# Optimization experiments

Measured on AMD Instinct MI355X. Metric: run time of the kernel, lower is better.

The kernel has to match this reference:

```python
import jax, jax.numpy as jnp
import numpy as np

N = 100000   # nodes
E = 800000   # undirected (unique) edges; directed count = 2*E
DV = 128; DE = 16; DH = 128; DO = 128
G = 64       # graphs in batch


def setup_inputs() -> dict:
    key = jax.random.key(0)
    ks = jax.random.split(key, 8)
    x = jax.random.normal(ks[0], (N, DV), jnp.float32)
    edge_index = jax.random.randint(ks[1], (2, 2 * E), 0, N, dtype=jnp.int32)
    edge_attr = jax.random.normal(ks[2], (E, DE), jnp.float32)
    batch = jnp.sort(jax.random.randint(ks[3], (N,), 0, G, dtype=jnp.int32))
    s = lambda k, shp, fan: jax.random.normal(k, shp, jnp.float32) / np.sqrt(fan)
    W_gcn = s(ks[4], (DV, DH), DV); b_gcn = jnp.zeros((DH,), jnp.float32)
    W_le = s(ks[5], (DE, DH), DE); b_le = jnp.zeros((DH,), jnp.float32)
    W_lin = s(ks[6], (2 * DH, DH), 2 * DH); b_lin = jnp.zeros((DH,), jnp.float32)
    W_out = s(ks[7], (DH, DO), DH); b_out = jnp.zeros((DO,), jnp.float32)
    return dict(x=x, edge_index=edge_index, edge_attr=edge_attr, batch=batch,
                W_gcn=W_gcn, b_gcn=b_gcn, W_le=W_le, b_le=b_le,
                W_lin=W_lin, b_lin=b_lin, W_out=W_out, b_out=b_out)


def reference(x, edge_index, edge_attr, batch,
              W_gcn, b_gcn, W_le, b_le, W_lin, b_lin, W_out, b_out):
    n = x.shape[0]
    loop = jnp.arange(n, dtype=edge_index.dtype)
    src = jnp.concatenate([edge_index[0], loop])  # [2E+N] with self loops
    dst = jnp.concatenate([edge_index[1], loop])

    # ---- GCNConv: symmetric norm, self-loops, lin then aggregate, + bias ----
    xw = x @ W_gcn                                      # [N, DH]
    ones_e = jnp.ones(src.shape[0], jnp.float32)
    deg = jax.ops.segment_sum(ones_e, dst, num_segments=n)  # >=1 via self loops
    dinv = jax.lax.rsqrt(deg)
    norm = dinv[src] * dinv[dst]                        # [2E+N]
    h = jax.ops.segment_sum(norm[:, None] * xw[src], dst, num_segments=n) + b_gcn
    h = jax.nn.relu(h)

    # ---- EdgeGCN: duplicate edge_attr per direction, self-loop attr = ones ----
    ea2 = jnp.repeat(edge_attr, 2, axis=0)              # [2E, DE] interleaved
    ea_full = jnp.concatenate([ea2, jnp.ones((n, edge_attr.shape[1]), jnp.float32)])
    edge_feat = ea_full @ W_le + b_le                   # [2E+N, DH]
    x_j = h[src]                                        # gather source node feats
    msg = jnp.concatenate([x_j, edge_feat], axis=-1) @ W_lin + b_lin
    h2 = jax.ops.segment_sum(msg, dst, num_segments=n)  # aggr='add'
    h2 = jax.nn.relu(h2)

    # ---- global mean pool + final linear ----
    cnt = jax.ops.segment_sum(jnp.ones(n, jnp.float32), batch, num_segments=G)
    pooled = jax.ops.segment_sum(h2, batch, num_segments=G) / jnp.maximum(cnt, 1.0)[:, None]
    return pooled @ W_out + b_out                       # [G, DO]
```

## Files before the change

kernel.cpp:

```cpp
#include <hip/hip_runtime.h>
#include <hip/hip_bf16.h>
#include <cstddef>

typedef unsigned int  u32;
typedef unsigned short u16;
typedef __attribute__((ext_vector_type(8))) short short8;
typedef __attribute__((ext_vector_type(4))) float f32x4;
typedef __attribute__((ext_vector_type(2))) float f32x2;

#define DV 128
#define DH 128
#define DE 16
#define DO 128
#define PSUB 32

__device__ inline float bf_lo(u32 u){ return __uint_as_float(u << 16); }
__device__ inline float bf_hi(u32 u){ return __uint_as_float(u & 0xFFFF0000u); }
__device__ inline u32 fpack2(float a, float b){
  u32 ua = __float_as_uint(a), ub = __float_as_uint(b);
  ua += 0x7FFFu + ((ua >> 16) & 1u);
  ub += 0x7FFFu + ((ub >> 16) & 1u);
  return (ua >> 16) | (ub & 0xFFFF0000u);
}
__device__ inline u16 f2bf(float a){
  u32 ua = __float_as_uint(a); ua += 0x7FFFu + ((ua >> 16) & 1u); return (u16)(ua >> 16);
}

__device__ inline void acc_fp8(u32 s, float& a0, float& a1, float& a2, float& a3){
  f32x2 lo = __builtin_amdgcn_cvt_pk_f32_fp8((int)s, false);
  f32x2 hi = __builtin_amdgcn_cvt_pk_f32_fp8((int)s, true);
  a0 += lo.x; a1 += lo.y; a2 += hi.x; a3 += hi.y;
}
__device__ inline u32 pack_fp8(float a0, float a1, float a2, float a3){
  int o = __builtin_amdgcn_cvt_pk_fp8_f32(a0, a1, 0, false);
  o = __builtin_amdgcn_cvt_pk_fp8_f32(a2, a3, o, true);
  return (u32)o;
}

__global__ void k_init(int* cnt, int n){
  int v = blockIdx.x * blockDim.x + threadIdx.x;
  if (v < n) cnt[v] = 0;
}
__global__ void k_count(const int* dst, int* cnt, int* rank, int e2){
  int j = blockIdx.x * blockDim.x + threadIdx.x;
  if (j < e2) rank[j] = atomicAdd(&cnt[dst[j]], 1);
}
__global__ __launch_bounds__(256) void k_scan1(const int* cnt, int* partial, int* bsums, int n){
  __shared__ int lds[256];
  int t = threadIdx.x;
  int base = blockIdx.x * 1024 + t * 4;
  int v0=0,v1=0,v2=0,v3=0;
  if (base + 3 < n){ int4 q = *(const int4*)(cnt + base); v0=q.x; v1=q.y; v2=q.z; v3=q.w; }
  else {
    if (base + 0 < n) v0 = cnt[base];
    if (base + 1 < n) v1 = cnt[base+1];
    if (base + 2 < n) v2 = cnt[base+2];
  }
  v0 = (v0 + 7) & ~7; v1 = (v1 + 7) & ~7; v2 = (v2 + 7) & ~7; v3 = (v3 + 7) & ~7;
  v1 += v0; v2 += v1; v3 += v2;
  lds[t] = v3; __syncthreads();
  for (int off = 1; off < 256; off <<= 1){
    int x = (t >= off) ? lds[t - off] : 0;
    __syncthreads();
    lds[t] += x;
    __syncthreads();
  }
  int add = (t > 0) ? lds[t - 1] : 0;
  if (base + 3 < n){
    int4 q; q.x = v0+add; q.y = v1+add; q.z = v2+add; q.w = v3+add;
    *(int4*)(partial + base) = q;
  } else {
    if (base + 0 < n) partial[base]   = v0 + add;
    if (base + 1 < n) partial[base+1] = v1 + add;
    if (base + 2 < n) partial[base+2] = v2 + add;
  }
  if (t == 255) bsums[blockIdx.x] = lds[255];
}
__global__ void k_scan2(const int* bsums, int* bexc, int nb){
  __shared__ int lds[128];
  int t = threadIdx.x;
  lds[t] = (t < nb) ? bsums[t] : 0;
  __syncthreads();
  for (int off = 1; off < 128; off <<= 1){
    int x = (t >= off) ? lds[t - off] : 0;
    __syncthreads();
    lds[t] += x;
    __syncthreads();
  }
  if (t < nb) bexc[t] = (t > 0) ? lds[t - 1] : 0;
}
__global__ void k_scan3(const int* partial, const int* bexc, int* row_ptr, int n){
  int i = blockIdx.x * blockDim.x + threadIdx.x;
  if (i < n) row_ptr[i + 1] = partial[i] + bexc[i >> 10];
  if (i == 0) row_ptr[0] = 0;
}
__global__ void k_prep(const int* cnt, float* dinv, float* degf, int n){
  int v = blockIdx.x * blockDim.x + threadIdx.x;
  if (v < n){
    float c = (float)(cnt[v] + 1);
    dinv[v] = rsqrtf(c);
    degf[v] = c;
  }
}
__global__ void k_scatter(const int* src, const int* dst, const int* rank,
                          const int* row_ptr, int2* ce, int e2){
  int j = blockIdx.x * blockDim.x + threadIdx.x;
  if (j < e2){
    int d = dst[j];
    int pos = row_ptr[d] + rank[j];
    ce[pos] = make_int2(src[j], j);
  }
}
__global__ void k_pad(const int* row_ptr, const int* cnt, int2* ce,
                      u32* xws_zrow, u32* h_zrow, int n){
  int v = blockIdx.x * blockDim.x + threadIdx.x;
  if (v < n){
    int s = row_ptr[v] + cnt[v], e = row_ptr[v + 1];
    for (int i = s; i < e; ++i) ce[i] = make_int2(n, 0);
  }
  if (blockIdx.x == 0 && threadIdx.x < 32){
    xws_zrow[threadIdx.x] = 0u;
    h_zrow[threadIdx.x] = 0u;
  }
}

__global__ __launch_bounds__(128) void k_wcombo(const float* W_lin, const float* b_lin,
                                                const float* W_le, const float* b_le, float* Wfull){
  int r = blockIdx.x, c = threadIdx.x;
  if (r < DH){
    Wfull[r * DH + c] = W_lin[r * DH + c];
  } else if (r < DH + DE){
    int i = r - DH;
    float acc = 0.f;
    #pragma unroll 8
    for (int k = 0; k < DH; k += 4){
      float4 wl = *(const float4*)(W_le + i * DH + k);
      acc += wl.x * W_lin[(size_t)(DH + k    ) * DH + c];
      acc += wl.y * W_lin[(size_t)(DH + k + 1) * DH + c];
      acc += wl.z * W_lin[(size_t)(DH + k + 2) * DH + c];
      acc += wl.w * W_lin[(size_t)(DH + k + 3) * DH + c];
    }
    Wfull[r * DH + c] = acc;
  } else if (r == 144){
    float acc = b_lin[c];
    #pragma unroll 8
    for (int k = 0; k < DH; k += 4){
      float4 bl = *(const float4*)(b_le + k);
      acc += bl.x * W_lin[(size_t)(DH + k    ) * DH + c];
      acc += bl.y * W_lin[(size_t)(DH + k + 1) * DH + c];
      acc += bl.z * W_lin[(size_t)(DH + k + 2) * DH + c];
      acc += bl.w * W_lin[(size_t)(DH + k + 3) * DH + c];
    }
    Wfull[r * DH + c] = acc;
  } else {
    Wfull[r * DH + c] = 0.f;
  }
}

template<int K, bool RELU, bool ABF16, bool SCALE, bool OFP8>
__global__ __launch_bounds__(256) void k_gemm_mfma(const void* Ap, const float* W, u32* outb,
                                                   const float* scale, int M){
  constexpr int SA = K + 8;
  constexpr int CS = 136;
  __shared__ u16 Wt[128 * SA];
  __shared__ u16 At[64 * SA];
  int tid = threadIdx.x;
  int row0 = blockIdx.x * 64;

  {
    int c = tid & 127, half = tid >> 7;
    for (int g = half; g < K / 8; g += 2){
      int k0 = g * 8;
      float w0 = W[(size_t)(k0+0)*128 + c], w1 = W[(size_t)(k0+1)*128 + c];
      float w2 = W[(size_t)(k0+2)*128 + c], w3 = W[(size_t)(k0+3)*128 + c];
      float w4 = W[(size_t)(k0+4)*128 + c], w5 = W[(size_t)(k0+5)*128 + c];
      float w6 = W[(size_t)(k0+6)*128 + c], w7 = W[(size_t)(k0+7)*128 + c];
      uint4 pk;
      pk.x = fpack2(w0, w1); pk.y = fpack2(w2, w3);
      pk.z = fpack2(w4, w5); pk.w = fpack2(w6, w7);
      *(uint4*)&Wt[c * SA + k0] = pk;
    }
  }
  constexpr int CH = K / 8;
  for (int idx = tid; idx < 64 * CH; idx += 256){
    int r = idx / CH, ch = idx - r * CH;
    int gr = row0 + r; if (gr > M - 1) gr = M - 1;
    uint4 pk;
    if (ABF16){
      pk = *(const uint4*)((const u16*)Ap + (size_t)gr * K + ch * 8);
    } else {
      const float* A = (const float*)Ap + (size_t)gr * K + ch * 8;
      float4 q0 = *(const float4*)A;
      float4 q1 = *(const float4*)(A + 4);
      pk.x = fpack2(q0.x, q0.y); pk.y = fpack2(q0.z, q0.w);
      pk.z = fpack2(q1.x, q1.y); pk.w = fpack2(q1.z, q1.w);
    }
    *(uint4*)&At[r * SA + ch * 8] = pk;
  }
  __syncthreads();

  int l = tid & 63, w = tid >> 6;
  int m = l & 15, quad = l >> 4;
  f32x4 acc[8];
  #pragma unroll
  for (int ct = 0; ct < 8; ++ct) acc[ct] = (f32x4){0.f, 0.f, 0.f, 0.f};
  #pragma unroll
  for (int ks = 0; ks < K; ks += 32){
    short8 av = *(const short8*)&At[(w * 16 + m) * SA + ks + quad * 8];
    #pragma unroll
    for (int ct = 0; ct < 8; ++ct){
      short8 bv = *(const short8*)&Wt[(ct * 16 + m) * SA + ks + quad * 8];
      acc[ct] = __builtin_amdgcn_mfma_f32_16x16x32_bf16(av, bv, acc[ct], 0, 0, 0);
    }
  }
  __syncthreads();

  u16* Ct = At;
  float sc[4];
  if (SCALE){
    #pragma unroll
    for (int r = 0; r < 4; ++r){
      int gr = row0 + w * 16 + quad * 4 + r;
      sc[r] = scale[gr < M ? gr : (M - 1)];
    }
  }
  #pragma unroll
  for (int ct = 0; ct < 8; ++ct){
    #pragma unroll
    for (int r = 0; r < 4; ++r){
      float vv = acc[ct][r];
      if (SCALE) vv *= sc[r];
      if (RELU)  vv = fmaxf(vv, 0.f);
      Ct[(w * 16 + quad * 4 + r) * CS + ct * 16 + m] = f2bf(vv);
    }
  }
  __syncthreads();
  if (OFP8){
    for (int idx = tid; idx < 64 * 16; idx += 256){
      int r = idx >> 4, c8 = idx & 15;
      int gr = row0 + r;
      if (gr < M){
        uint4 qv = *(const uint4*)&Ct[r * CS + c8 * 8];
        uint2 ov;
        ov.x = (u32)__builtin_amdgcn_cvt_pk_fp8_f32(bf_lo(qv.y), bf_hi(qv.y),
               __builtin_amdgcn_cvt_pk_fp8_f32(bf_lo(qv.x), bf_hi(qv.x), 0, false), true);
        ov.y = (u32)__builtin_amdgcn_cvt_pk_fp8_f32(bf_lo(qv.w), bf_hi(qv.w),
               __builtin_amdgcn_cvt_pk_fp8_f32(bf_lo(qv.z), bf_hi(qv.z), 0, false), true);
        *(uint2*)(outb + (size_t)gr * 32 + c8 * 2) = ov;
      }
    }
  } else {
    for (int idx = tid; idx < 64 * 16; idx += 256){
      int r = idx >> 4, ch = idx & 15;
      int gr = row0 + r;
      if (gr < M){
        uint4 q = *(const uint4*)&Ct[r * CS + ch * 8];
        *(uint4*)(outb + (size_t)gr * 64 + ch * 4) = q;
      }
    }
  }
}

__global__ __launch_bounds__(256) void k_phase1(const u32* xws8, const int* row_ptr, const int2* ce,
                                                const float* dinv, const float* b_gcn, u32* h8, int n){
  int lane = threadIdx.x & 63;
  int ln = lane & 31;
  int v = blockIdx.x * 8 + ((threadIdx.x >> 6) << 1) + (lane >> 5);
  if (v >= n) return;
  u32 sp = xws8[(size_t)v * 32 + ln];
  float a0 = 0.f, a1 = 0.f, a2 = 0.f, a3 = 0.f;
  acc_fp8(sp, a0, a1, a2, a3);
  int e0 = row_ptr[v], e1 = row_ptr[v + 1];
  int i = e0;
  u32 q0=0,q1=0,q2=0,q3=0,q4=0,q5=0,q6=0,q7=0;
  if (i < e1){
    const int4* cp = (const int4*)(ce + i);
    int4 A = cp[0], B = cp[1], C = cp[2], D = cp[3];
    q0 = xws8[(size_t)A.x * 32 + ln]; q1 = xws8[(size_t)A.z * 32 + ln];
    q2 = xws8[(size_t)B.x * 32 + ln]; q3 = xws8[(size_t)B.z * 32 + ln];
    q4 = xws8[(size_t)C.x * 32 + ln]; q5 = xws8[(size_t)C.z * 32 + ln];
    q6 = xws8[(size_t)D.x * 32 + ln]; q7 = xws8[(size_t)D.z * 32 + ln];
  }
  for (; i + 8 < e1; i += 8){
    const int4* cp2 = (const int4*)(ce + i + 8);
    int4 A = cp2[0], B = cp2[1], C = cp2[2], D = cp2[3];
    u32 p0 = xws8[(size_t)A.x * 32 + ln], p1 = xws8[(size_t)A.z * 32 + ln];
    u32 p2 = xws8[(size_t)B.x * 32 + ln], p3 = xws8[(size_t)B.z * 32 + ln];
    u32 p4 = xws8[(size_t)C.x * 32 + ln], p5 = xws8[(size_t)C.z * 32 + ln];
    u32 p6 = xws8[(size_t)D.x * 32 + ln], p7 = xws8[(size_t)D.z * 32 + ln];
    acc_fp8(q0, a0, a1, a2, a3); acc_fp8(q1, a0, a1, a2, a3);
    acc_fp8(q2, a0, a1, a2, a3); acc_fp8(q3, a0, a1, a2, a3);
    acc_fp8(q4, a0, a1, a2, a3); acc_fp8(q5, a0, a1, a2, a3);
    acc_fp8(q6, a0, a1, a2, a3); acc_fp8(q7, a0, a1, a2, a3);
    q0=p0; q1=p1; q2=p2; q3=p3; q4=p4; q5=p5; q6=p6; q7=p7;
  }
  if (i < e1){
    acc_fp8(q0, a0, a1, a2, a3); acc_fp8(q1, a0, a1, a2, a3);
    acc_fp8(q2, a0, a1, a2, a3); acc_fp8(q3, a0, a1, a2, a3);
    acc_fp8(q4, a0, a1, a2, a3); acc_fp8(q5, a0, a1, a2, a3);
    acc_fp8(q6, a0, a1, a2, a3); acc_fp8(q7, a0, a1, a2, a3);
  }
  float dv = dinv[v];
  float4 bg = *(const float4*)(b_gcn + ln * 4);
  a0 = fmaxf(fmaf(dv, a0, bg.x), 0.f);
  a1 = fmaxf(fmaf(dv, a1, bg.y), 0.f);
  a2 = fmaxf(fmaf(dv, a2, bg.z), 0.f);
  a3 = fmaxf(fmaf(dv, a3, bg.w), 0.f);
  h8[(size_t)v * 32 + ln] = pack_fp8(a0, a1, a2, a3);
}

__global__ __launch_bounds__(256) void k_phase2(const u32* h8, const int* row_ptr, const int2* ce,
                                                const float* edge_attr, const float* degf,
                                                u16* A2b, int n){
  int lane = threadIdx.x & 63;
  int ln = lane & 31;
  int half = lane >> 5;
  int v = blockIdx.x * 8 + ((threadIdx.x >> 6) << 1) + half;
  if (v >= n) return;
  u32 sp = h8[(size_t)v * 32 + ln];
  float a0 = 0.f, a1 = 0.f, a2 = 0.f, a3 = 0.f;
  acc_fp8(sp, a0, a1, a2, a3);
  float es = 0.f;
  int ch = ln & 15, grp = ln >> 4;
  int e0 = row_ptr[v], e1 = row_ptr[v + 1];
  int i = e0;
  u32 q0=0,q1=0,q2=0,q3=0,q4=0,q5=0,q6=0,q7=0;
  int4 A = {0,0,0,0}, B = {0,0,0,0}, C = {0,0,0,0}, D = {0,0,0,0};
  if (i < e1){
    const int4* cp = (const int4*)(ce + i);
    A = cp[0]; B = cp[1]; C = cp[2]; D = cp[3];
    q0 = h8[(size_t)A.x * 32 + ln]; q1 = h8[(size_t)A.z * 32 + ln];
    q2 = h8[(size_t)B.x * 32 + ln]; q3 = h8[(size_t)B.z * 32 + ln];
    q4 = h8[(size_t)C.x * 32 + ln]; q5 = h8[(size_t)C.z * 32 + ln];
    q6 = h8[(size_t)D.x * 32 + ln]; q7 = h8[(size_t)D.z * 32 + ln];
  }
  for (; i + 8 < e1; i += 8){
    const int4* cp2 = (const int4*)(ce + i + 8);
    int4 A2 = cp2[0], B2 = cp2[1], C2 = cp2[2], D2 = cp2[3];
    int s0x = grp ? C.x : A.x, s0y = grp ? C.y : A.y;
    int s1x = grp ? C.z : A.z, s1y = grp ? C.w : A.w;
    int s2x = grp ? D.x : B.x, s2y = grp ? D.y : B.y;
    int s3x = grp ? D.z : B.z, s3y = grp ? D.w : B.w;
    float v0 = edge_attr[(size_t)(s0y >> 1) * DE + ch];
    float v1 = edge_attr[(size_t)(s1y >> 1) * DE + ch];
    float v2 = edge_attr[(size_t)(s2y >> 1) * DE + ch];
    float v3 = edge_attr[(size_t)(s3y >> 1) * DE + ch];
    u32 p0 = h8[(size_t)A2.x * 32 + ln], p1 = h8[(size_t)A2.z * 32 + ln];
    u32 p2 = h8[(size_t)B2.x * 32 + ln], p3 = h8[(size_t)B2.z * 32 + ln];
    u32 p4 = h8[(size_t)C2.x * 32 + ln], p5 = h8[(size_t)C2.z * 32 + ln];
    u32 p6 = h8[(size_t)D2.x * 32 + ln], p7 = h8[(size_t)D2.z * 32 + ln];
    acc_fp8(q0, a0, a1, a2, a3); acc_fp8(q1, a0, a1, a2, a3);
    acc_fp8(q2, a0, a1, a2, a3); acc_fp8(q3, a0, a1, a2, a3);
    acc_fp8(q4, a0, a1, a2, a3); acc_fp8(q5, a0, a1, a2, a3);
    acc_fp8(q6, a0, a1, a2, a3); acc_fp8(q7, a0, a1, a2, a3);
    es = fmaf((s0x != n) ? 1.f : 0.f, v0, es);
    es = fmaf((s1x != n) ? 1.f : 0.f, v1, es);
    es = fmaf((s2x != n) ? 1.f : 0.f, v2, es);
    es = fmaf((s3x != n) ? 1.f : 0.f, v3, es);
    q0=p0; q1=p1; q2=p2; q3=p3; q4=p4; q5=p5; q6=p6; q7=p7;
    A=A2; B=B2; C=C2; D=D2;
  }
  if (i < e1){
    int s0x = grp ? C.x : A.x, s0y = grp ? C.y : A.y;
    int s1x = grp ? C.z : A.z, s1y = grp ? C.w : A.w;
    int s2x = grp ? D.x : B.x, s2y = grp ? D.y : B.y;
    int s3x = grp ? D.z : B.z, s3y = grp ? D.w : B.w;
    float v0 = edge_attr[(size_t)(s0y >> 1) * DE + ch];
    float v1 = edge_attr[(size_t)(s1y >> 1) * DE + ch];
    float v2 = edge_attr[(size_t)(s2y >> 1) * DE + ch];
    float v3 = edge_attr[(size_t)(s3y >> 1) * DE + ch];
    acc_fp8(q0, a0, a1, a2, a3); acc_fp8(q1, a0, a1, a2, a3);
    acc_fp8(q2, a0, a1, a2, a3); acc_fp8(q3, a0, a1, a2, a3);
    acc_fp8(q4, a0, a1, a2, a3); acc_fp8(q5, a0, a1, a2, a3);
    acc_fp8(q6, a0, a1, a2, a3); acc_fp8(q7, a0, a1, a2, a3);
    es = fmaf((s0x != n) ? 1.f : 0.f, v0, es);
    es = fmaf((s1x != n) ? 1.f : 0.f, v1, es);
    es = fmaf((s2x != n) ? 1.f : 0.f, v2, es);
    es = fmaf((s3x != n) ? 1.f : 0.f, v3, es);
  }
  es += __shfl_xor(es, 16);
  float c0v = __shfl(es, half * 32 + (ln & 7) * 2);
  float c1v = __shfl(es, half * 32 + (ln & 7) * 2 + 1);
  u32* rowp = (u32*)(A2b + (size_t)v * 160);
  uint2 o; o.x = fpack2(a0, a1); o.y = fpack2(a2, a3);
  *(uint2*)(rowp + ln * 2) = o;
  if (ln < 8){
    rowp[64 + ln] = fpack2(c0v + 1.0f, c1v + 1.0f);
  } else if (ln < 16){
    rowp[64 + ln] = (ln == 8) ? (u32)f2bf(degf[v]) : 0u;
  }
}

__global__ void k_starts(const int* batch, int* start, int n, int g){
  int v = blockIdx.x * blockDim.x + threadIdx.x;
  if (v >= n) return;
  int b = batch[v];
  int prev = (v == 0) ? -1 : batch[v - 1];
  for (int q = prev + 1; q <= b; ++q) start[q] = v;
  if (v == n - 1){ for (int q = b + 1; q <= g; ++q) start[q] = n; }
}
__global__ __launch_bounds__(256) void k_pool_a(const u32* h2_b, const int* start, float* partialp){
  __shared__ float2 red[256];
  int g = blockIdx.x >> 5;
  int s = blockIdx.x & (PSUB - 1);
  int s0 = start[g], s1 = start[g + 1];
  int tid = threadIdx.x;
  int cu = tid & 63, rr = tid >> 6;
  float ax = 0.f, ay = 0.f;
  for (int r = s0 + s * 4 + rr; r < s1; r += PSUB * 4){
    u32 q = h2_b[(size_t)r * 64 + cu];
    ax += bf_lo(q); ay += bf_hi(q);
  }
  red[tid] = make_float2(ax, ay);
  __syncthreads();
  if (rr == 0){
    #pragma unroll
    for (int p = 1; p < 4; p++){ float2 o = red[cu + (p << 6)]; ax += o.x; ay += o.y; }
    *(float2*)(partialp + (size_t)blockIdx.x * 128 + cu * 2) = make_float2(ax, ay);
  }
}
__global__ __launch_bounds__(128) void k_poolb_final(const float* partialp, const int* start,
                                                     const float* W_out, const float* b_out,
                                                     float* out){
  __shared__ float pl[DH];
  int g = blockIdx.x, c = threadIdx.x;
  float sum = 0.f;
  #pragma unroll 4
  for (int s = 0; s < PSUB; ++s) sum += partialp[((size_t)g * PSUB + s) * 128 + c];
  int cntg = start[g + 1] - start[g]; if (cntg < 1) cntg = 1;
  pl[c] = sum / (float)cntg;
  __syncthreads();
  float acc = b_out[c];
  for (int k = 0; k < DH; ++k) acc += pl[k] * W_out[k * DO + c];
  out[g * DO + c] = acc;
}

extern "C" void kernel_launch(void* const* d_in, const int* in_sizes, int n_in,
                              void* d_out, int out_size, void* d_ws, size_t ws_size,
                              hipStream_t stream){
  const float* x         = (const float*)d_in[0];
  const int*   edge_index= (const int*)  d_in[1];
  const float* edge_attr = (const float*)d_in[2];
  const int*   batch     = (const int*)  d_in[3];
  const float* W_gcn     = (const float*)d_in[4];
  const float* b_gcn     = (const float*)d_in[5];
  const float* W_le      = (const float*)d_in[6];
  const float* b_le      = (const float*)d_in[7];
  const float* W_lin     = (const float*)d_in[8];
  const float* b_lin     = (const float*)d_in[9];
  const float* W_out     = (const float*)d_in[10];
  const float* b_out     = (const float*)d_in[11];
  float* out = (float*)d_out;

  const int n  = in_sizes[0] / DV;
  const int e2 = in_sizes[1] / 2;
  const int g  = out_size / DO;
  const int* srcp = edge_index;
  const int* dstp = edge_index + e2;
  const int e2pad = e2 + 7 * n + 8;

  char* ws = (char*)d_ws;
  size_t off = 0;
  auto alloc = [&](size_t bytes) -> char* {
    char* p = ws + off; off = (off + bytes + 255) & ~(size_t)255; return p;
  };

  int*   cnt     = (int*)  alloc((size_t)n * 4);
  int*   row_ptr = (int*)  alloc((size_t)(n + 1) * 4);
  int*   rank    = (int*)  alloc((size_t)e2 * 4);
  int*   partial = (int*)  alloc((size_t)n * 4);
  int*   bsums   = (int*)  alloc(512);
  int*   bexc    = (int*)  alloc(512);
  float* dinv    = (float*)alloc((size_t)n * 4);
  float* degf    = (float*)alloc((size_t)n * 4);
  int*   startg  = (int*)  alloc((size_t)(g + 1) * 4);
  float* partialp= (float*)alloc((size_t)g * PSUB * 128 * 4);
  float* Wfull   = (float*)alloc(160 * DH * 4);
  u32*   h8      = (u32*)  alloc((size_t)(n + 1) * 128);
  int2*  ce      = (int2*) alloc((size_t)e2pad * 8);
  u32*   h2_b    = (u32*)  alloc((size_t)n * 64 * 4);
  size_t szXW = (size_t)(n + 1) * 128, szA2 = (size_t)n * 160 * 2;
  char* regionA = alloc(szA2 > szXW ? szA2 : szXW);
  u32* xws8 = (u32*)regionA;
  u16* A2b  = (u16*)regionA;

  const int nb1024 = (n + 1023) / 1024;

  k_init   <<<(n + 255) / 256, 256, 0, stream>>>(cnt, n);
  k_count  <<<(e2 + 255) / 256, 256, 0, stream>>>(dstp, cnt, rank, e2);
  k_scan1  <<<nb1024, 256, 0, stream>>>(cnt, partial, bsums, n);
  k_scan2  <<<1, 128, 0, stream>>>(bsums, bexc, nb1024);
  k_scan3  <<<(n + 255) / 256, 256, 0, stream>>>(partial, bexc, row_ptr, n);
  k_prep   <<<(n + 255) / 256, 256, 0, stream>>>(cnt, dinv, degf, n);
  k_scatter<<<(e2 + 255) / 256, 256, 0, stream>>>(srcp, dstp, rank, row_ptr, ce, e2);
  k_pad    <<<(n + 255) / 256, 256, 0, stream>>>(row_ptr, cnt, ce,
                                                 xws8 + (size_t)n * 32, h8 + (size_t)n * 32, n);
  k_wcombo <<<160, 128, 0, stream>>>(W_lin, b_lin, W_le, b_le, Wfull);

  k_gemm_mfma<DV, false, false, true, true><<<(n + 63) / 64, 256, 0, stream>>>(x, W_gcn, xws8, dinv, n);
  k_phase1 <<<(n + 7) / 8, 256, 0, stream>>>(xws8, row_ptr, ce, dinv, b_gcn, h8, n);
  k_phase2 <<<(n + 7) / 8, 256, 0, stream>>>(h8, row_ptr, ce, edge_attr, degf, A2b, n);
  k_gemm_mfma<160, true, true, false, false><<<(n + 63) / 64, 256, 0, stream>>>(A2b, Wfull, h2_b, (const float*)nullptr, n);

  k_starts      <<<(n + 255) / 256, 256, 0, stream>>>(batch, startg, n, g);
  k_pool_a      <<<g * PSUB, 256, 0, stream>>>(h2_b, startg, partialp);
  k_poolb_final <<<g, 128, 0, stream>>>(partialp, startg, W_out, b_out, out);
}
```

Baseline: 416.4 us.

## Fuse pooling into second GEMM, split CSR arrays, bf16 edge attrs, merge prep kernels

Several changes land together. The global mean-pool sums are now accumulated directly from the second MFMA GEMM's accumulators with atomics, which removes the h2 write-back and the separate pooling kernels. The CSR edge list is split into a pre-shifted source index array and an edge-id array, read with nontemporal vector loads. Edge attributes are converted to bf16 during the count pass so phase2 gathers half the bytes. Several small setup kernels (scan3/prep/starts and scatter/pad) are merged to cut launch count, at the cost of float atomic ordering nondeterminism and an extra edge_attr pass during counting.

```diff
diff --git a/kernel.cpp b/kernel.cpp
--- a/kernel.cpp
+++ b/kernel.cpp
@@ -7,12 +7,12 @@
 typedef __attribute__((ext_vector_type(8))) short short8;
 typedef __attribute__((ext_vector_type(4))) float f32x4;
 typedef __attribute__((ext_vector_type(2))) float f32x2;
+typedef __attribute__((ext_vector_type(4))) int i32x4;
 
 #define DV 128
 #define DH 128
 #define DE 16
 #define DO 128
-#define PSUB 32
 
 __device__ inline float bf_lo(u32 u){ return __uint_as_float(u << 16); }
 __device__ inline float bf_hi(u32 u){ return __uint_as_float(u & 0xFFFF0000u); }
@@ -37,13 +37,27 @@
   return (u32)o;
 }
 
-__global__ void k_init(int* cnt, int n){
+__device__ inline i32x4 ld_nt4(const int* p){
+  return __builtin_nontemporal_load((const i32x4*)p);
+}
+
+__global__ void k_init(int* cnt, float* poolp, int n, int pn){
   int v = blockIdx.x * blockDim.x + threadIdx.x;
   if (v < n) cnt[v] = 0;
-}
-__global__ void k_count(const int* dst, int* cnt, int* rank, int e2){
+  if (v < pn) poolp[v] = 0.f;
+}
+__global__ void k_count(const int* dst, const float* edge_attr, int* cnt, int* rank,
+                        u32* ea_pack, int e2){
   int j = blockIdx.x * blockDim.x + threadIdx.x;
-  if (j < e2) rank[j] = atomicAdd(&cnt[dst[j]], 1);
+  if (j < e2){
+    rank[j] = atomicAdd(&cnt[dst[j]], 1);
+    float4 f0 = *(const float4*)(edge_attr + (size_t)j * 8);
+    float4 f1 = *(const float4*)(edge_attr + (size_t)j * 8 + 4);
+    uint4 o;
+    o.x = fpack2(f0.x, f0.y); o.y = fpack2(f0.z, f0.w);
+    o.z = fpack2(f1.x, f1.y); o.w = fpack2(f1.z, f1.w);
+    *(uint4*)(ea_pack + (size_t)j * 4) = o;
+  }
 }
 __global__ __launch_bounds__(256) void k_scan1(const int* cnt, int* partial, int* bsums, int n){
   __shared__ int lds[256];
@@ -89,38 +103,41 @@
   }
   if (t < nb) bexc[t] = (t > 0) ? lds[t - 1] : 0;
 }
-__global__ void k_scan3(const int* partial, const int* bexc, int* row_ptr, int n){
+__global__ void k_scan3f(const int* partial, const int* bexc, int* row_ptr,
+                         const int* cnt, float* dinv, float* degf,
+                         const int* batch, int* startg, int n, int g){
   int i = blockIdx.x * blockDim.x + threadIdx.x;
-  if (i < n) row_ptr[i + 1] = partial[i] + bexc[i >> 10];
-  if (i == 0) row_ptr[0] = 0;
-}
-__global__ void k_prep(const int* cnt, float* dinv, float* degf, int n){
-  int v = blockIdx.x * blockDim.x + threadIdx.x;
-  if (v < n){
-    float c = (float)(cnt[v] + 1);
-    dinv[v] = rsqrtf(c);
-    degf[v] = c;
-  }
-}
-__global__ void k_scatter(const int* src, const int* dst, const int* rank,
-                          const int* row_ptr, int2* ce, int e2){
+  if (i < n){
+    row_ptr[i + 1] = partial[i] + bexc[i >> 10];
+    if (i == 0) row_ptr[0] = 0;
+    float c = (float)(cnt[i] + 1);
+    dinv[i] = rsqrtf(c);
+    degf[i] = c;
+    int b = batch[i];
+    int prev = (i == 0) ? -1 : batch[i - 1];
+    for (int q = prev + 1; q <= b; ++q) startg[q] = i;
+    if (i == n - 1){ for (int q = b + 1; q <= g; ++q) startg[q] = n; }
+  }
+}
+__global__ void k_scatterpad(const int* src, const int* dst, const int* rank,
+                             const int* row_ptr, const int* cnt,
+                             int* ce_src, int* ce_eid,
+                             u32* xws_zrow, u32* h_zrow, int e2, int n){
   int j = blockIdx.x * blockDim.x + threadIdx.x;
   if (j < e2){
     int d = dst[j];
     int pos = row_ptr[d] + rank[j];
-    ce[pos] = make_int2(src[j], j);
-  }
-}
-__global__ void k_pad(const int* row_ptr, const int* cnt, int2* ce,
-                      u32* xws_zrow, u32* h_zrow, int n){
-  int v = blockIdx.x * blockDim.x + threadIdx.x;
-  if (v < n){
-    int s = row_ptr[v] + cnt[v], e = row_ptr[v + 1];
-    for (int i = s; i < e; ++i) ce[i] = make_int2(n, 0);
-  }
-  if (blockIdx.x == 0 && threadIdx.x < 32){
-    xws_zrow[threadIdx.x] = 0u;
-    h_zrow[threadIdx.x] = 0u;
+    ce_src[pos] = src[j] << 5;
+    ce_eid[pos] = j >> 1;
+  }
+  if (j < n){
+    int s = row_ptr[j] + cnt[j], e = row_ptr[j + 1];
+    int nm = n << 5;
+    for (int i = s; i < e; ++i){ ce_src[i] = nm; ce_eid[i] = 0; }
+  }
+  if (j < 32){
+    xws_zrow[j] = 0u;
+    h_zrow[j] = 0u;
   }
 }
 
@@ -157,9 +174,10 @@
   }
 }
 
-template<int K, bool RELU, bool ABF16, bool SCALE, bool OFP8>
+template<int K, bool RELU, bool ABF16, bool SCALE, bool OFP8, bool POOL>
 __global__ __launch_bounds__(256) void k_gemm_mfma(const void* Ap, const float* W, u32* outb,
-                                                   const float* scale, int M){
+                                                   const float* scale, int M,
+                                                   const int* batchp, float* poolp){
   constexpr int SA = K + 8;
   constexpr int CS = 136;
   __shared__ u16 Wt[128 * SA];
@@ -214,6 +232,45 @@
     }
   }
   __syncthreads();
+
+  if (POOL){
+    float* ps = (float*)At;
+    int rbase = w * 16 + quad * 4;
+    int g0 = batchp[row0];
+    int glast = batchp[(row0 + 63 < M) ? (row0 + 63) : (M - 1)];
+    if (g0 == glast){
+      #pragma unroll
+      for (int ct = 0; ct < 8; ++ct){
+        float s = 0.f;
+        #pragma unroll
+        for (int r = 0; r < 4; ++r){
+          float vv = fmaxf(acc[ct][r], 0.f);
+          if (row0 + rbase + r < M) s += vv;
+        }
+        s += __shfl_xor(s, 16);
+        s += __shfl_xor(s, 32);
+        if (quad == 0) ps[w * 128 + ct * 16 + m] = s;
+      }
+      __syncthreads();
+      if (tid < 128){
+        float t = ps[tid] + ps[128 + tid] + ps[256 + tid] + ps[384 + tid];
+        atomicAdd(&poolp[g0 * DO + tid], t);
+      }
+    } else {
+      #pragma unroll
+      for (int ct = 0; ct < 8; ++ct){
+        #pragma unroll
+        for (int r = 0; r < 4; ++r){
+          int row = row0 + rbase + r;
+          if (row < M){
+            float vv = fmaxf(acc[ct][r], 0.f);
+            atomicAdd(&poolp[batchp[row] * DO + ct * 16 + m], vv);
+          }
+        }
+      }
+    }
+    return;
+  }
 
   u16* Ct = At;
   float sc[4];
@@ -261,7 +318,7 @@
   }
 }
 
-__global__ __launch_bounds__(256) void k_phase1(const u32* xws8, const int* row_ptr, const int2* ce,
+__global__ __launch_bounds__(256) void k_phase1(const u32* xws8, const int* row_ptr, const int* ce_src,
                                                 const float* dinv, const float* b_gcn, u32* h8, int n){
   int lane = threadIdx.x & 63;
   int ln = lane & 31;
@@ -274,20 +331,18 @@
   int i = e0;
   u32 q0=0,q1=0,q2=0,q3=0,q4=0,q5=0,q6=0,q7=0;
   if (i < e1){
-    const int4* cp = (const int4*)(ce + i);
-    int4 A = cp[0], B = cp[1], C = cp[2], D = cp[3];
-    q0 = xws8[(size_t)A.x * 32 + ln]; q1 = xws8[(size_t)A.z * 32 + ln];
-    q2 = xws8[(size_t)B.x * 32 + ln]; q3 = xws8[(size_t)B.z * 32 + ln];
-    q4 = xws8[(size_t)C.x * 32 + ln]; q5 = xws8[(size_t)C.z * 32 + ln];
-    q6 = xws8[(size_t)D.x * 32 + ln]; q7 = xws8[(size_t)D.z * 32 + ln];
+    i32x4 A = ld_nt4(ce_src + i);
+    i32x4 B = ld_nt4(ce_src + i + 4);
+    q0 = xws8[A.x + ln]; q1 = xws8[A.y + ln]; q2 = xws8[A.z + ln]; q3 = xws8[A.w + ln];
+    q4 = xws8[B.x + ln]; q5 = xws8[B.y + ln]; q6 = xws8[B.z + ln]; q7 = xws8[B.w + ln];
   }
   for (; i + 8 < e1; i += 8){
-    const int4* cp2 = (const int4*)(ce + i + 8);
-    int4 A = cp2[0], B = cp2[1], C = cp2[2], D = cp2[3];
-    u32 p0 = xws8[(size_t)A.x * 32 + ln], p1 = xws8[(size_t)A.z * 32 + ln];
-    u32 p2 = xws8[(size_t)B.x * 32 + ln], p3 = xws8[(size_t)B.z * 32 + ln];
-    u32 p4 = xws8[(size_t)C.x * 32 + ln], p5 = xws8[(size_t)C.z * 32 + ln];
-    u32 p6 = xws8[(size_t)D.x * 32 + ln], p7 = xws8[(size_t)D.z * 32 + ln];
+    i32x4 A = ld_nt4(ce_src + i + 8);
+    i32x4 B = ld_nt4(ce_src + i + 12);
+    u32 p0 = xws8[A.x + ln], p1 = xws8[A.y + ln];
+    u32 p2 = xws8[A.z + ln], p3 = xws8[A.w + ln];
+    u32 p4 = xws8[B.x + ln], p5 = xws8[B.y + ln];
+    u32 p6 = xws8[B.z + ln], p7 = xws8[B.w + ln];
     acc_fp8(q0, a0, a1, a2, a3); acc_fp8(q1, a0, a1, a2, a3);
     acc_fp8(q2, a0, a1, a2, a3); acc_fp8(q3, a0, a1, a2, a3);
     acc_fp8(q4, a0, a1, a2, a3); acc_fp8(q5, a0, a1, a2, a3);
@@ -309,8 +364,9 @@
   h8[(size_t)v * 32 + ln] = pack_fp8(a0, a1, a2, a3);
 }
 
-__global__ __launch_bounds__(256) void k_phase2(const u32* h8, const int* row_ptr, const int2* ce,
-                                                const float* edge_attr, const float* degf,
+__global__ __launch_bounds__(256) void k_phase2(const u32* h8, const int* row_ptr,
+                                                const int* ce_src, const int* ce_eid,
+                                                const u16* ea_bf, const float* degf,
                                                 u16* A2b, int n){
   int lane = threadIdx.x & 63;
   int ln = lane & 31;
@@ -322,61 +378,60 @@
   acc_fp8(sp, a0, a1, a2, a3);
   float es = 0.f;
   int ch = ln & 15, grp = ln >> 4;
+  int nmark = n << 5;
   int e0 = row_ptr[v], e1 = row_ptr[v + 1];
   int i = e0;
   u32 q0=0,q1=0,q2=0,q3=0,q4=0,q5=0,q6=0,q7=0;
-  int4 A = {0,0,0,0}, B = {0,0,0,0}, C = {0,0,0,0}, D = {0,0,0,0};
+  i32x4 As = (i32x4)0, Bs = (i32x4)0, Ae = (i32x4)0, Be = (i32x4)0;
   if (i < e1){
-    const int4* cp = (const int4*)(ce + i);
-    A = cp[0]; B = cp[1]; C = cp[2]; D = cp[3];
-    q0 = h8[(size_t)A.x * 32 + ln]; q1 = h8[(size_t)A.z * 32 + ln];
-    q2 = h8[(size_t)B.x * 32 + ln]; q3 = h8[(size_t)B.z * 32 + ln];
-    q4 = h8[(size_t)C.x * 32 + ln]; q5 = h8[(size_t)C.z * 32 + ln];
-    q6 = h8[(size_t)D.x * 32 + ln]; q7 = h8[(size_t)D.z * 32 + ln];
+    As = ld_nt4(ce_src + i);     Bs = ld_nt4(ce_src + i + 4);
+    Ae = ld_nt4(ce_eid + i);     Be = ld_nt4(ce_eid + i + 4);
+    q0 = h8[As.x + ln]; q1 = h8[As.y + ln]; q2 = h8[As.z + ln]; q3 = h8[As.w + ln];
+    q4 = h8[Bs.x + ln]; q5 = h8[Bs.y + ln]; q6 = h8[Bs.z + ln]; q7 = h8[Bs.w + ln];
   }
   for (; i + 8 < e1; i += 8){
-    const int4* cp2 = (const int4*)(ce + i + 8);
-    int4 A2 = cp2[0], B2 = cp2[1], C2 = cp2[2], D2 = cp2[3];
-    int s0x = grp ? C.x : A.x, s0y = grp ? C.y : A.y;
-    int s1x = grp ? C.z : A.z, s1y = grp ? C.w : A.w;
-    int s2x = grp ? D.x : B.x, s2y = grp ? D.y : B.y;
-    int s3x = grp ? D.z : B.z, s3y = grp ? D.w : B.w;
-    float v0 = edge_attr[(size_t)(s0y >> 1) * DE + ch];
-    float v1 = edge_attr[(size_t)(s1y >> 1) * DE + ch];
-    float v2 = edge_attr[(size_t)(s2y >> 1) * DE + ch];
-    float v3 = edge_attr[(size_t)(s3y >> 1) * DE + ch];
-    u32 p0 = h8[(size_t)A2.x * 32 + ln], p1 = h8[(size_t)A2.z * 32 + ln];
-    u32 p2 = h8[(size_t)B2.x * 32 + ln], p3 = h8[(size_t)B2.z * 32 + ln];
-    u32 p4 = h8[(size_t)C2.x * 32 + ln], p5 = h8[(size_t)C2.z * 32 + ln];
-    u32 p6 = h8[(size_t)D2.x * 32 + ln], p7 = h8[(size_t)D2.z * 32 + ln];
+    i32x4 As2 = ld_nt4(ce_src + i + 8);   i32x4 Bs2 = ld_nt4(ce_src + i + 12);
+    i32x4 Ae2 = ld_nt4(ce_eid + i + 8);   i32x4 Be2 = ld_nt4(ce_eid + i + 12);
+    int s0x = grp ? Bs.x : As.x, s0e = grp ? Be.x : Ae.x;
+    int s1x = grp ? Bs.y : As.y, s1e = grp ? Be.y : Ae.y;
+    int s2x = grp ? Bs.z : As.z, s2e = grp ? Be.z : Ae.z;
+    int s3x = grp ? Bs.w : As.w, s3e = grp ? Be.w : Ae.w;
+    float v0 = bf_lo((u32)ea_bf[(size_t)s0e * 16 + ch]);
+    float v1 = bf_lo((u32)ea_bf[(size_t)s1e * 16 + ch]);
+    float v2 = bf_lo((u32)ea_bf[(size_t)s2e * 16 + ch]);
+    float v3 = bf_lo((u32)ea_bf[(size_t)s3e * 16 + ch]);
+    u32 p0 = h8[As2.x + ln], p1 = h8[As2.y + ln];
+    u32 p2 = h8[As2.z + ln], p3 = h8[As2.w + ln];
+    u32 p4 = h8[Bs2.x + ln], p5 = h8[Bs2.y + ln];
+    u32 p6 = h8[Bs2.z + ln], p7 = h8[Bs2.w + ln];
     acc_fp8(q0, a0, a1, a2, a3); acc_fp8(q1, a0, a1, a2, a3);
     acc_fp8(q2, a0, a1, a2, a3); acc_fp8(q3, a0, a1, a2, a3);
     acc_fp8(q4, a0, a1, a2, a3); acc_fp8(q5, a0, a1, a2, a3);
     acc_fp8(q6, a0, a1, a2, a3); acc_fp8(q7, a0, a1, a2, a3);
-    es = fmaf((s0x != n) ? 1.f : 0.f, v0, es);
-    es = fmaf((s1x != n) ? 1.f : 0.f, v1, es);
-    es = fmaf((s2x != n) ? 1.f : 0.f, v2, es);
-    es = fmaf((s3x != n) ? 1.f : 0.f, v3, es);
+    es = fmaf((s0x != nmark) ? 1.f : 0.f, v0, es);
+    es = fmaf((s1x != nmark) ? 1.f : 0.f, v1, es);
+    es = fmaf((s2x != nmark) ? 1.f : 0.f, v2, es);
+    es = fmaf((s3x != nmark) ? 1.f : 0.f, v3, es);
     q0=p0; q1=p1; q2=p2; q3=p3; q4=p4; q5=p5; q6=p6; q7=p7;
-    A=A2; B=B2; C=C2; D=D2;
+    As=As2; Bs=Bs2; Ae=Ae2; Be=Be2;
   }
   if (i < e1){
-    int s0x = grp ? C.x : A.x, s0y = grp ? C.y : A.y;
-    int s1x = grp ? C.z : A.z, s1y = grp ? C.w : A.w;
-    int s2x = grp ? D.x : B.x, s2y = grp ? D.y : B.y;
-    int s3x = grp ? D.z : B.z, s3y = grp ? D.w : B.w;
-    float v0 = edge_attr[(size_t)(s0y >> 1) * DE + ch];
-    float v1 = edge_attr[(size_t)(s1y >> 1) * DE + ch];
-    float v2 = edge_attr[(size_t)(s2y >> 1) * DE + ch];
-    float v3 = edge_attr[(size_t)(s3y >> 1) * DE + ch];
+    int s0x = grp ? Bs.x : As.x, s0e = grp ? Be.x : Ae.x;
+    int s1x = grp ? Bs.y : As.y, s1e = grp ? Be.y : Ae.y;
+    int s2x = grp ? Bs.z : As.z, s2e = grp ? Be.z : Ae.z;
+    int s3x = grp ? Bs.w : As.w, s3e = grp ? Be.w : Ae.w;
+    float v0 = bf_lo((u32)ea_bf[(size_t)s0e * 16 + ch]);
+    float v1 = bf_lo((u32)ea_bf[(size_t)s1e * 16 + ch]);
+    float v2 = bf_lo((u32)ea_bf[(size_t)s2e * 16 + ch]);
+    float v3 = bf_lo((u32)ea_bf[(size_t)s3e * 16 + ch]);
     acc_fp8(q0, a0, a1, a2, a3); acc_fp8(q1, a0, a1, a2, a3);
     acc_fp8(q2, a0, a1, a2, a3); acc_fp8(q3, a0, a1, a2, a3);
     acc_fp8(q4, a0, a1, a2, a3); acc_fp8(q5, a0, a1, a2, a3);
     acc_fp8(q6, a0, a1, a2, a3); acc_fp8(q7, a0, a1, a2, a3);
-    es = fmaf((s0x != n) ? 1.f : 0.f, v0, es);
-    es = fmaf((s1x != n) ? 1.f : 0.f, v1, es);
-    es = fmaf((s2x != n) ? 1.f : 0.f, v2, es);
-    es = fmaf((s3x != n) ? 1.f : 0.f, v3, es);
+    es = fmaf((s0x != nmark) ? 1.f : 0.f, v0, es);
+    es = fmaf((s1x != nmark) ? 1.f : 0.f, v1, es);
+    es = fmaf((s2x != nmark) ? 1.f : 0.f, v2, es);
+    es = fmaf((s3x != nmark) ? 1.f : 0.f, v3, es);
   }
   es += __shfl_xor(es, 16);
   float c0v = __shfl(es, half * 32 + (ln & 7) * 2);
@@ -391,44 +446,13 @@
   }
 }
 
-__global__ void k_starts(const int* batch, int* start, int n, int g){
-  int v = blockIdx.x * blockDim.x + threadIdx.x;
-  if (v >= n) return;
-  int b = batch[v];
-  int prev = (v == 0) ? -1 : batch[v - 1];
-  for (int q = prev + 1; q <= b; ++q) start[q] = v;
-  if (v == n - 1){ for (int q = b + 1; q <= g; ++q) start[q] = n; }
-}
-__global__ __launch_bounds__(256) void k_pool_a(const u32* h2_b, const int* start, float* partialp){
-  __shared__ float2 red[256];
-  int g = blockIdx.x >> 5;
-  int s = blockIdx.x & (PSUB - 1);
-  int s0 = start[g], s1 = start[g + 1];
-  int tid = threadIdx.x;
-  int cu = tid & 63, rr = tid >> 6;
-  float ax = 0.f, ay = 0.f;
-  for (int r = s0 + s * 4 + rr; r < s1; r += PSUB * 4){
-    u32 q = h2_b[(size_t)r * 64 + cu];
-    ax += bf_lo(q); ay += bf_hi(q);
-  }
-  red[tid] = make_float2(ax, ay);
-  __syncthreads();
-  if (rr == 0){
-    #pragma unroll
-    for (int p = 1; p < 4; p++){ float2 o = red[cu + (p << 6)]; ax += o.x; ay += o.y; }
-    *(float2*)(partialp + (size_t)blockIdx.x * 128 + cu * 2) = make_float2(ax, ay);
-  }
-}
-__global__ __launch_bounds__(128) void k_poolb_final(const float* partialp, const int* start,
+__global__ __launch_bounds__(128) void k_poolb_final(const float* poolp, const int* start,
                                                      const float* W_out, const float* b_out,
                                                      float* out){
   __shared__ float pl[DH];
   int g = blockIdx.x, c = threadIdx.x;
-  float sum = 0.f;
-  #pragma unroll 4
-  for (int s = 0; s < PSUB; ++s) sum += partialp[((size_t)g * PSUB + s) * 128 + c];
   int cntg = start[g + 1] - start[g]; if (cntg < 1) cntg = 1;
-  pl[c] = sum / (float)cntg;
+  pl[c] = poolp[g * DO + c] / (float)cntg;
   __syncthreads();
   float acc = b_out[c];
   for (int k = 0; k < DH; ++k) acc += pl[k] * W_out[k * DO + c];
@@ -474,11 +498,12 @@
   float* dinv    = (float*)alloc((size_t)n * 4);
   float* degf    = (float*)alloc((size_t)n * 4);
   int*   startg  = (int*)  alloc((size_t)(g + 1) * 4);
-  float* partialp= (float*)alloc((size_t)g * PSUB * 128 * 4);
+  float* poolp   = (float*)alloc((size_t)g * DO * 4);
   float* Wfull   = (float*)alloc(160 * DH * 4);
   u32*   h8      = (u32*)  alloc((size_t)(n + 1) * 128);
-  int2*  ce      = (int2*) alloc((size_t)e2pad * 8);
-  u32*   h2_b    = (u32*)  alloc((size_t)n * 64 * 4);
+  int*   ce_src  = (int*)  alloc((size_t)e2pad * 4);
+  int*   ce_eid  = (int*)  alloc((size_t)e2pad * 4);
+  u32*   ea_bf   = (u32*)  alloc((size_t)e2 * 16);
   size_t szXW = (size_t)(n + 1) * 128, szA2 = (size_t)n * 160 * 2;
   char* regionA = alloc(szA2 > szXW ? szA2 : szXW);
   u32* xws8 = (u32*)regionA;
@@ -486,23 +511,25 @@
 
   const int nb1024 = (n + 1023) / 1024;
 
-  k_init   <<<(n + 255) / 256, 256, 0, stream>>>(cnt, n);
-  k_count  <<<(e2 + 255) / 256, 256, 0, stream>>>(dstp, cnt, rank, e2);
-  k_scan1  <<<nb1024, 256, 0, stream>>>(cnt, partial, bsums, n);
-  k_scan2  <<<1, 128, 0, stream>>>(bsums, bexc, nb1024);
-  k_scan3  <<<(n + 255) / 256, 256, 0, stream>>>(partial, bexc, row_ptr, n);
-  k_prep   <<<(n + 255) / 256, 256, 0, stream>>>(cnt, dinv, degf, n);
-  k_scatter<<<(e2 + 255) / 256, 256, 0, stream>>>(srcp, dstp, rank, row_ptr, ce, e2);
-  k_pad    <<<(n + 255) / 256, 256, 0, stream>>>(row_ptr, cnt, ce,
-                                                 xws8 + (size_t)n * 32, h8 + (size_t)n * 32, n);
-  k_wcombo <<<160, 128, 0, stream>>>(W_lin, b_lin, W_le, b_le, Wfull);
-
-  k_gemm_mfma<DV, false, false, true, true><<<(n + 63) / 64, 256, 0, stream>>>(x, W_gcn, xws8, dinv, n);
-  k_phase1 <<<(n + 7) / 8, 256, 0, stream>>>(xws8, row_ptr, ce, dinv, b_gcn, h8, n);
-  k_phase2 <<<(n + 7) / 8, 256, 0, stream>>>(h8, row_ptr, ce, edge_attr, degf, A2b, n);
-  k_gemm_mfma<160, true, true, false, false><<<(n + 63) / 64, 256, 0, stream>>>(A2b, Wfull, h2_b, (const float*)nullptr, n);
-
-  k_starts      <<<(n + 255) / 256, 256, 0, stream>>>(batch, startg, n, g);
-  k_pool_a      <<<g * PSUB, 256, 0, stream>>>(h2_b, startg, partialp);
-  k_poolb_final <<<g, 128, 0, stream>>>(partialp, startg, W_out, b_out, out);
-}
+  k_init      <<<(n + 255) / 256, 256, 0, stream>>>(cnt, poolp, n, g * DO);
+  k_count     <<<(e2 + 255) / 256, 256, 0, stream>>>(dstp, edge_attr, cnt, rank, ea_bf, e2);
+  k_scan1     <<<nb1024, 256, 0, stream>>>(cnt, partial, bsums, n);
+  k_scan2     <<<1, 128, 0, stream>>>(bsums, bexc, nb1024);
+  k_scan3f    <<<(n + 255) / 256, 256, 0, stream>>>(partial, bexc, row_ptr, cnt, dinv, degf,
+                                                    batch, startg, n, g);
+  k_scatterpad<<<(e2 + 255) / 256, 256, 0, stream>>>(srcp, dstp, rank, row_ptr, cnt,
+                                                     ce_src, ce_eid,
+                                                     xws8 + (size_t)n * 32, h8 + (size_t)n * 32,
+                                                     e2, n);
+  k_wcombo    <<<160, 128, 0, stream>>>(W_lin, b_lin, W_le, b_le, Wfull);
+
+  k_gemm_mfma<DV, false, false, true, true, false>
+      <<<(n + 63) / 64, 256, 0, stream>>>(x, W_gcn, xws8, dinv, n, nullptr, nullptr);
+  k_phase1    <<<(n + 7) / 8, 256, 0, stream>>>(xws8, row_ptr, ce_src, dinv, b_gcn, h8, n);
+  k_phase2    <<<(n + 7) / 8, 256, 0, stream>>>(h8, row_ptr, ce_src, ce_eid,
+                                                (const u16*)ea_bf, degf, A2b, n);
+  k_gemm_mfma<160, true, true, false, false, true>
+      <<<(n + 63) / 64, 256, 0, stream>>>(A2b, Wfull, (u32*)nullptr, (const float*)nullptr,
+                                          n, batch, poolp);
+  k_poolb_final<<<g, 128, 0, stream>>>(poolp, startg, W_out, b_out, out);
+}
```

Result: slower. 463.7 us (+11.4%).
